# Kernel optimization log

Hardware: AMD Instinct MI355X
Metric: run time of the kernel (lower is better)

## Reference

```python
import jax, jax.numpy as jnp
import numpy as np

ALPHA, GAMMA, EPS = 0.25, 2.0, 1e-8
COST_CLASS, COST_BBOX, COST_GIOU = 2.0, 5.0, 2.0


def box_cxcywh_to_xyxy(b):
    cx, cy, w, h = jnp.split(b, 4, axis=-1)
    return jnp.concatenate([cx - 0.5 * w, cy - 0.5 * h, cx + 0.5 * w, cy + 0.5 * h], axis=-1)


def setup_inputs() -> dict:
    key = jax.random.key(0)
    k1, k2, k3, k4 = jax.random.split(key, 4)
    bs, Q, C, T = 16, 900, 80, 1600
    return {
        "pred_logits": jax.random.normal(k1, (bs, Q, C), jnp.float32),
        "pred_boxes": jax.random.uniform(k2, (bs, Q, 4), jnp.float32),
        "tgt_labels": jax.random.randint(k3, (T,), 0, C),
        "tgt_boxes": jax.random.uniform(k4, (T, 4), jnp.float32),
        "g_size": 3,
    }


def reference(pred_logits, pred_boxes, tgt_labels, tgt_boxes, g_size):
    bs, Q, _ = pred_logits.shape
    # focal classification cost (use_focal=True path)
    p = jax.nn.sigmoid(pred_logits.reshape(bs * Q, -1))  # [N, C]
    neg = (1.0 - ALPHA) * p ** GAMMA * (-jnp.log(1.0 - p + EPS))
    pos = ALPHA * (1.0 - p) ** GAMMA * (-jnp.log(p + EPS))
    cost_class = (pos - neg)[:, tgt_labels]  # [N, T]
    # L1 box cost (cdist p=1)
    out_bbox = pred_boxes.reshape(bs * Q, 4)
    cost_bbox = jnp.abs(out_bbox[:, None, :] - tgt_bbox_b(tgt_boxes)).sum(-1)  # [N, T]
    # GIoU cost
    b1 = box_cxcywh_to_xyxy(out_bbox)  # [N, 4]
    b2 = box_cxcywh_to_xyxy(tgt_boxes)  # [T, 4]
    area1 = (b1[:, 2] - b1[:, 0]) * (b1[:, 3] - b1[:, 1])
    area2 = (b2[:, 2] - b2[:, 0]) * (b2[:, 3] - b2[:, 1])
    lt = jnp.maximum(b1[:, None, :2], b2[None, :, :2])
    rb = jnp.minimum(b1[:, None, 2:], b2[None, :, 2:])
    wh = jnp.clip(rb - lt, 0.0)
    inter = wh[..., 0] * wh[..., 1]
    union = area1[:, None] + area2[None, :] - inter
    iou = inter / union
    elt = jnp.minimum(b1[:, None, :2], b2[None, :, :2])
    erb = jnp.maximum(b1[:, None, 2:], b2[None, :, 2:])
    ewh = jnp.clip(erb - elt, 0.0)
    earea = ewh[..., 0] * ewh[..., 1]
    giou = iou - (earea - union) / earea
    # weighted total cost, then group reduction (note: original names it Cmin but takes max over the group dim)
    Cmat = COST_BBOX * cost_bbox + COST_CLASS * cost_class + COST_GIOU * (-giou)
    Cmin = Cmat.reshape(bs, Q // g_size, g_size, -1).max(axis=2)  # [bs, Q//g, T]
    return Cmin


def tgt_bbox_b(tgt_boxes):
    return tgt_boxes[None, :, :]
```

## Files before the change

kernel.cpp:

```cpp
#include <hip/hip_runtime.h>

#define ALPHA 0.25f
#define EPS   1e-8f

constexpr int BS = 16;
constexpr int QN = 900;
constexpr int CN = 80;
constexpr int GS = 3;
constexpr int QG_PER_BLOCK = 4;
constexpr int ROWS = QG_PER_BLOCK * GS;
constexpr int NT_THREADS = 256;
constexpr int TSPLIT = 2;

__global__ __launch_bounds__(NT_THREADS) void fused_cost_kernel(
    const float* __restrict__ pred_logits,
    const float* __restrict__ pred_boxes,
    const int*   __restrict__ tgt_labels,
    const float* __restrict__ tgt_boxes,
    float*       __restrict__ out,
    int T)
{
    __shared__ __align__(16) float s_cc_t[CN * ROWS];

    const int tid = threadIdx.x;
    const int qg0 = blockIdx.y * QG_PER_BLOCK;
    const int b   = blockIdx.z;
    const int n0  = b * QN + qg0 * GS;

    const float* lg0 = pred_logits + (size_t)n0 * CN;
    if (tid < (ROWS * CN) / 4) {
        const float4 x4 = ((const float4*)lg0)[tid];
        const int base = tid * 4;
        const int r = base / CN;
        const int c = base - r * CN;
        const float xs[4] = { x4.x, x4.y, x4.z, x4.w };
        #pragma unroll
        for (int i = 0; i < 4; ++i) {
            float p = __fdividef(1.0f, 1.0f + __expf(-xs[i]));
            float omp = 1.0f - p;
            float pos = ALPHA * omp * omp * (-__logf(p + EPS));
            float neg = (1.0f - ALPHA) * p * p * (-__logf(omp + EPS));
            s_cc_t[(c + i) * ROWS + r] = pos - neg;
        }
    }

    float Px0[ROWS], Py0[ROWS], Px1[ROWS], Py1[ROWS];
    float Pw[ROWS], Ph[ROWS], Pa[ROWS];
    #pragma unroll
    for (int r = 0; r < ROWS; ++r) {
        const float4 pb = ((const float4*)pred_boxes)[n0 + r];
        Pw[r] = pb.z;  Ph[r] = pb.w;  Pa[r] = pb.z * pb.w;
        Px0[r] = pb.x - 0.5f * pb.z;  Py0[r] = pb.y - 0.5f * pb.w;
        Px1[r] = pb.x + 0.5f * pb.z;  Py1[r] = pb.y + 0.5f * pb.w;
    }
    __syncthreads();

    const int tChunk = T / TSPLIT;
    const int t0 = blockIdx.x * tChunk;
    const int tEnd = t0 + tChunk;
    const int qgTotal = QN / GS;
    const size_t outBase = (size_t)(b * qgTotal + qg0) * T;

    int t = t0 + tid;
    if (t >= tEnd) return;
    float4 tr = ((const float4*)tgt_boxes)[t];
    int    lab = tgt_labels[t];

    while (true) {
        const int  tn    = t + NT_THREADS;
        const bool more  = tn < tEnd;
        const int  tsafe = more ? tn : t;
        const float4 trn  = ((const float4*)tgt_boxes)[tsafe];
        const int    labn = tgt_labels[tsafe];

        const float4* ccp = (const float4*)&s_cc_t[lab * ROWS];
        const float4 c0 = ccp[0], c1 = ccp[1], c2 = ccp[2];
        const float ccv[ROWS] = { c0.x, c0.y, c0.z, c0.w,
                                  c1.x, c1.y, c1.z, c1.w,
                                  c2.x, c2.y, c2.z, c2.w };

        const float tx0 = tr.x - 0.5f * tr.z, ty0 = tr.y - 0.5f * tr.w;
        const float tx1 = tr.x + 0.5f * tr.z, ty1 = tr.y + 0.5f * tr.w;
        const float ta  = tr.z * tr.w;

        #pragma unroll
        for (int j = 0; j < QG_PER_BLOCK; ++j) {
            float m = -3.402823466e+38f;
            #pragma unroll
            for (int g = 0; g < GS; ++g) {
                const int i = j * GS + g;

                const float dx0 = Px0[i] - tx0;
                const float dx1 = Px1[i] - tx1;
                const float dy0 = Py0[i] - ty0;
                const float dy1 = Py1[i] - ty1;

                const float l1 = fmaf(0.5f,
                    fabsf(dx0 + dx1) + fabsf(dy0 + dy1),
                    fabsf(Pw[i] - tr.z) + fabsf(Ph[i] - tr.w));

                const float abx = fabsf(dx0) + fabsf(dx1);
                const float aby = fabsf(dy0) + fabsf(dy1);
                const float sx  = Pw[i] + tr.z;
                const float sy  = Ph[i] + tr.w;
                const float IW  = fmaxf(sx - abx, 0.0f);
                const float IH  = fmaxf(sy - aby, 0.0f);
                const float inter4 = IW * IH;
                const float earea4 = (sx + abx) * (sy + aby);

                const float uni = fmaf(-0.25f, inter4, Pa[i] + ta);

                const float num = fmaf(0.5f * inter4, earea4, 8.0f * uni * uni);
                const float den = uni * earea4;
                const float g2  = __fdividef(num, den);

                const float cost = fmaf(5.0f, l1, fmaf(2.0f, ccv[i], 2.0f - g2));
                m = fmaxf(m, cost);
            }
            out[outBase + (size_t)j * T + t] = m;
        }

        if (!more) break;
        t = tn; tr = trn; lab = labn;
    }
}

extern "C" void kernel_launch(void* const* d_in, const int* in_sizes, int n_in,
                              void* d_out, int out_size, void* d_ws, size_t ws_size,
                              hipStream_t stream) {
    const float* pred_logits = (const float*)d_in[0];
    const float* pred_boxes  = (const float*)d_in[1];
    const int*   tgt_labels  = (const int*)d_in[2];
    const float* tgt_boxes   = (const float*)d_in[3];

    const int T = in_sizes[2];
    float* out = (float*)d_out;

    dim3 grid(TSPLIT, (QN / GS) / QG_PER_BLOCK, BS);
    fused_cost_kernel<<<grid, NT_THREADS, 0, stream>>>(
        pred_logits, pred_boxes, tgt_labels, tgt_boxes, out, T);
}
```

Before: 100.9 us.

## Drop target split, use 320-thread blocks with packed float2 math and nontemporal stores

Removes the two-way split of targets across blocks, so each block of 320 threads now covers all targets in five fixed iterations when T equals 1600. It adds a template specialisation with a compile-time trip count. The per-pair box arithmetic is rewritten with two-wide float vectors so the compiler can emit packed FP32 instructions. Outputs are written with nontemporal stores. Halving the grid means the logit sigmoid/log preprocessing is no longer duplicated per block, but it also reduces the number of blocks available for parallelism.

```diff
diff --git a/kernel.cpp b/kernel.cpp
--- a/kernel.cpp
+++ b/kernel.cpp
@@ -9,10 +9,19 @@
 constexpr int GS = 3;
 constexpr int QG_PER_BLOCK = 4;
 constexpr int ROWS = QG_PER_BLOCK * GS;
-constexpr int NT_THREADS = 256;
-constexpr int TSPLIT = 2;
+constexpr int NT_THREADS = 320;
 
-__global__ __launch_bounds__(NT_THREADS) void fused_cost_kernel(
+typedef float v2f __attribute__((ext_vector_type(2)));
+
+static __device__ __forceinline__ v2f vabs2(v2f a) {
+    return (v2f){ fabsf(a.x), fabsf(a.y) };
+}
+static __device__ __forceinline__ v2f vmax2(v2f a, v2f b) {
+    return (v2f){ fmaxf(a.x, b.x), fmaxf(a.y, b.y) };
+}
+
+template<int NITER>
+__global__ __launch_bounds__(NT_THREADS, 4) void fused_cost_kernel(
     const float* __restrict__ pred_logits,
     const float* __restrict__ pred_boxes,
     const int*   __restrict__ tgt_labels,
@@ -23,8 +32,8 @@
     __shared__ __align__(16) float s_cc_t[CN * ROWS];
 
     const int tid = threadIdx.x;
-    const int qg0 = blockIdx.y * QG_PER_BLOCK;
-    const int b   = blockIdx.z;
+    const int qg0 = blockIdx.x * QG_PER_BLOCK;
+    const int b   = blockIdx.y;
     const int n0  = b * QN + qg0 * GS;
 
     const float* lg0 = pred_logits + (size_t)n0 * CN;
@@ -44,34 +53,33 @@
         }
     }
 
-    float Px0[ROWS], Py0[ROWS], Px1[ROWS], Py1[ROWS];
-    float Pw[ROWS], Ph[ROWS], Pa[ROWS];
+    v2f P0[ROWS], PWH[ROWS];
+    float Pa[ROWS];
     #pragma unroll
     for (int r = 0; r < ROWS; ++r) {
         const float4 pb = ((const float4*)pred_boxes)[n0 + r];
-        Pw[r] = pb.z;  Ph[r] = pb.w;  Pa[r] = pb.z * pb.w;
-        Px0[r] = pb.x - 0.5f * pb.z;  Py0[r] = pb.y - 0.5f * pb.w;
-        Px1[r] = pb.x + 0.5f * pb.z;  Py1[r] = pb.y + 0.5f * pb.w;
+        PWH[r] = (v2f){ pb.z, pb.w };
+        P0[r]  = (v2f){ pb.x - 0.5f * pb.z, pb.y - 0.5f * pb.w };
+        Pa[r]  = pb.z * pb.w;
     }
     __syncthreads();
 
-    const int tChunk = T / TSPLIT;
-    const int t0 = blockIdx.x * tChunk;
-    const int tEnd = t0 + tChunk;
     const int qgTotal = QN / GS;
-    const size_t outBase = (size_t)(b * qgTotal + qg0) * T;
+    float* const o0 = out + (size_t)(b * qgTotal + qg0) * T;
+    const v2f Z2 = { 0.0f, 0.0f };
 
-    int t = t0 + tid;
-    if (t >= tEnd) return;
-    float4 tr = ((const float4*)tgt_boxes)[t];
-    int    lab = tgt_labels[t];
+    const int nIter = (NITER > 0) ? NITER : ((T + NT_THREADS - 1) / NT_THREADS);
 
-    while (true) {
-        const int  tn    = t + NT_THREADS;
-        const bool more  = tn < tEnd;
-        const int  tsafe = more ? tn : t;
-        const float4 trn  = ((const float4*)tgt_boxes)[tsafe];
-        const int    labn = tgt_labels[tsafe];
+    int t = tid;
+    int tl = (NITER > 0) ? t : ((t < T) ? t : (T - 1));
+    float4 tr  = ((const float4*)tgt_boxes)[tl];
+    int    lab = tgt_labels[tl];
+
+    for (int it = 0; it < nIter; ++it) {
+        const int tn = t + NT_THREADS;
+        const int tc = (tn < T) ? tn : tl;
+        const float4 trn  = ((const float4*)tgt_boxes)[tc];
+        const int    labn = tgt_labels[tc];
 
         const float4* ccp = (const float4*)&s_cc_t[lab * ROWS];
         const float4 c0 = ccp[0], c1 = ccp[1], c2 = ccp[2];
@@ -79,9 +87,11 @@
                                   c1.x, c1.y, c1.z, c1.w,
                                   c2.x, c2.y, c2.z, c2.w };
 
-        const float tx0 = tr.x - 0.5f * tr.z, ty0 = tr.y - 0.5f * tr.w;
-        const float tx1 = tr.x + 0.5f * tr.z, ty1 = tr.y + 0.5f * tr.w;
-        const float ta  = tr.z * tr.w;
+        const v2f T0  = (v2f){ tr.x - 0.5f * tr.z, tr.y - 0.5f * tr.w };
+        const v2f TWH = (v2f){ tr.z, tr.w };
+        const float ta = tr.z * tr.w;
+
+        const bool doWrite = (NITER > 0) || (t < T);
 
         #pragma unroll
         for (int j = 0; j < QG_PER_BLOCK; ++j) {
@@ -90,26 +100,20 @@
             for (int g = 0; g < GS; ++g) {
                 const int i = j * GS + g;
 
-                const float dx0 = Px0[i] - tx0;
-                const float dx1 = Px1[i] - tx1;
-                const float dy0 = Py0[i] - ty0;
-                const float dy1 = Py1[i] - ty1;
+                const v2f D0 = P0[i] - T0;
+                const v2f WD = PWH[i] - TWH;
+                const v2f D1 = D0 + WD;
+                const v2f AB = vabs2(D0) + vabs2(D1);
+                const v2f S  = PWH[i] + TWH;
+                const v2f IWH = vmax2(S - AB, Z2);
+                const v2f E  = S + AB;
+                const v2f DS = D0 + D1;
 
-                const float l1 = fmaf(0.5f,
-                    fabsf(dx0 + dx1) + fabsf(dy0 + dy1),
-                    fabsf(Pw[i] - tr.z) + fabsf(Ph[i] - tr.w));
-
-                const float abx = fabsf(dx0) + fabsf(dx1);
-                const float aby = fabsf(dy0) + fabsf(dy1);
-                const float sx  = Pw[i] + tr.z;
-                const float sy  = Ph[i] + tr.w;
-                const float IW  = fmaxf(sx - abx, 0.0f);
-                const float IH  = fmaxf(sy - aby, 0.0f);
-                const float inter4 = IW * IH;
-                const float earea4 = (sx + abx) * (sy + aby);
-
+                const float inter4 = IWH.x * IWH.y;
+                const float earea4 = E.x * E.y;
+                const float l1 = fmaf(0.5f, fabsf(DS.x) + fabsf(DS.y),
+                                            fabsf(WD.x) + fabsf(WD.y));
                 const float uni = fmaf(-0.25f, inter4, Pa[i] + ta);
-
                 const float num = fmaf(0.5f * inter4, earea4, 8.0f * uni * uni);
                 const float den = uni * earea4;
                 const float g2  = __fdividef(num, den);
@@ -117,11 +121,11 @@
                 const float cost = fmaf(5.0f, l1, fmaf(2.0f, ccv[i], 2.0f - g2));
                 m = fmaxf(m, cost);
             }
-            out[outBase + (size_t)j * T + t] = m;
+            if (doWrite)
+                __builtin_nontemporal_store(m, o0 + (size_t)j * T + t);
         }
 
-        if (!more) break;
-        t = tn; tr = trn; lab = labn;
+        t = tn; tl = tc; tr = trn; lab = labn;
     }
 }
 
@@ -136,7 +140,12 @@
     const int T = in_sizes[2];
     float* out = (float*)d_out;
 
-    dim3 grid(TSPLIT, (QN / GS) / QG_PER_BLOCK, BS);
-    fused_cost_kernel<<<grid, NT_THREADS, 0, stream>>>(
-        pred_logits, pred_boxes, tgt_labels, tgt_boxes, out, T);
+    dim3 grid((QN / GS) / QG_PER_BLOCK, BS);
+    if (T == NT_THREADS * 5) {
+        fused_cost_kernel<5><<<grid, NT_THREADS, 0, stream>>>(
+            pred_logits, pred_boxes, tgt_labels, tgt_boxes, out, T);
+    } else {
+        fused_cost_kernel<0><<<grid, NT_THREADS, 0, stream>>>(
+            pred_logits, pred_boxes, tgt_labels, tgt_boxes, out, T);
+    }
 }
```

Result: no change. 101.6 us (+0.7%).
